# Optimization experiments

Hardware: AMD Instinct MI355X
Metric: run time of the kernel (lower is better)

The kernel has to match this reference:

```python
import jax, jax.numpy as jnp
import numpy as np

N, E, P, D = 100000, 800000, 100000, 128

def setup_inputs() -> dict:
    key = jax.random.key(0)
    ks = jax.random.split(key, 24)
    def w(k, i, o):
        return jax.random.normal(k, (i, o), jnp.float32) * (1.0 / np.sqrt(i))
    inp = {
        'x': jax.random.normal(ks[0], (N, D), jnp.float32),
        'src': jax.random.randint(ks[1], (E,), 0, N, jnp.int32),
        'dst': jax.random.randint(ks[2], (E,), 0, N, jnp.int32),
        'pos_src': jax.random.randint(ks[3], (P,), 0, N, jnp.int32),
        'pos_dst': jax.random.randint(ks[4], (P,), 0, N, jnp.int32),
        'neg_src': jax.random.randint(ks[5], (P,), 0, N, jnp.int32),
        'neg_dst': jax.random.randint(ks[6], (P,), 0, N, jnp.int32),
        # SAGEConv params: fc_self, fc_neigh (+bias) per layer
        'Ws0': w(ks[7], D, D), 'Wn0': w(ks[8], D, D), 'b0': jnp.zeros((D,), jnp.float32),
        'Ws1': w(ks[9], D, D), 'Wn1': w(ks[10], D, D), 'b1': jnp.zeros((D,), jnp.float32),
        'Ws2': w(ks[11], D, D), 'Wn2': w(ks[12], D, D), 'b2': jnp.zeros((D,), jnp.float32),
        # predictor MLP: D->D->D->2
        'Wp0': w(ks[13], D, D), 'bp0': jnp.zeros((D,), jnp.float32),
        'Wp1': w(ks[14], D, D), 'bp1': jnp.zeros((D,), jnp.float32),
        'Wp2': w(ks[15], D, 2), 'bp2': jnp.zeros((2,), jnp.float32),
    }
    return inp

def _sage_layer(h, src, dst, n, Ws, Wn, b, act):
    # mean aggregation over in-neighbors (gather -> segment_sum -> divide)
    msum = jax.ops.segment_sum(h[src], dst, num_segments=n)      # [N, D]
    deg = jax.ops.segment_sum(jnp.ones_like(dst, jnp.float32), dst, num_segments=n)
    h_neigh = msum / jnp.maximum(deg, 1.0)[:, None]
    out = h @ Ws + h_neigh @ Wn + b
    return jax.nn.relu(out) if act else out

def _predict(hs, hd, Wp0, bp0, Wp1, bp1, Wp2, bp2):
    z = hs * hd
    z = jax.nn.relu(z @ Wp0 + bp0)
    z = jax.nn.relu(z @ Wp1 + bp1)
    return jax.nn.softmax(z @ Wp2 + bp2, axis=1)[:, 1]

def reference(x, src, dst, pos_src, pos_dst, neg_src, neg_dst,
              Ws0, Wn0, b0, Ws1, Wn1, b1, Ws2, Wn2, b2,
              Wp0, bp0, Wp1, bp1, Wp2, bp2):
    n = x.shape[0]
    h = _sage_layer(x, src, dst, n, Ws0, Wn0, b0, True)
    h = _sage_layer(h, src, dst, n, Ws1, Wn1, b1, True)
    h = _sage_layer(h, src, dst, n, Ws2, Wn2, b2, False)
    pos = _predict(h[pos_src], h[pos_dst], Wp0, bp0, Wp1, bp1, Wp2, bp2)
    neg = _predict(h[neg_src], h[neg_dst], Wp0, bp0, Wp1, bp1, Wp2, bp2)
    return (pos, neg)
```

## Files before the change

### kernel.cpp

```cpp
#include <hip/hip_runtime.h>
#include <cstdint>
#include <cstddef>
#include <cmath>

#define D 128

typedef short bf16x8 __attribute__((ext_vector_type(8)));
typedef float f32x4 __attribute__((ext_vector_type(4)));

__device__ __forceinline__ ushort f2b(float f) {
  uint x = __float_as_uint(f);
  uint r = ((x >> 16) & 1u) + 0x7fffu;
  return (ushort)((x + r) >> 16);
}
__device__ __forceinline__ float b2f(ushort u) {
  return __uint_as_float(((uint)u) << 16);
}

__global__ __launch_bounds__(256) void k_degree_p(const int* __restrict__ dst, int E,
    int* __restrict__ deg, float scale, int CE) {
  int part = blockIdx.x & 7, chunk = blockIdx.x >> 3;
  long base = (long)chunk * CE;
  for (int i = threadIdx.x; i < CE; i += 256) {
    long e = base + i;
    if (e < E) {
      int d = dst[e];
      int p = (int)((float)d * scale); if (p > 7) p = 7;
      if (p == part) atomicAdd(&deg[d], 1);
    }
  }
}

__global__ __launch_bounds__(256) void k_fill_p(const int* __restrict__ src,
    const int* __restrict__ dst, int E, int* __restrict__ cursor,
    int* __restrict__ csrc, float scale, int CE) {
  int part = blockIdx.x & 7, chunk = blockIdx.x >> 3;
  long base = (long)chunk * CE;
  for (int i = threadIdx.x; i < CE; i += 256) {
    long e = base + i;
    if (e < E) {
      int d = dst[e];
      int p = (int)((float)d * scale); if (p > 7) p = 7;
      if (p == part) {
        int s = src[e];
        int pos = atomicAdd(&cursor[d], 1);
        csrc[pos] = s;
      }
    }
  }
}

#define SCAN_T 256
#define SCAN_E 4
#define SCAN_CHUNK (SCAN_T * SCAN_E)

__global__ void k_scan_partial(const int* __restrict__ deg, int n, int* __restrict__ part) {
  __shared__ int s[SCAN_T];
  int base = blockIdx.x * SCAN_CHUNK;
  int sum = 0;
  for (int i = 0; i < SCAN_E; ++i) {
    int idx = base + (int)threadIdx.x * SCAN_E + i;
    if (idx < n) sum += deg[idx];
  }
  s[threadIdx.x] = sum; __syncthreads();
  for (int ofs = SCAN_T / 2; ofs > 0; ofs >>= 1) {
    if ((int)threadIdx.x < ofs) s[threadIdx.x] += s[threadIdx.x + ofs];
    __syncthreads();
  }
  if (threadIdx.x == 0) part[blockIdx.x] = s[0];
}

__global__ void k_scan_part_ex(int* __restrict__ part, int nb) {
  __shared__ int s[1024];
  int v = ((int)threadIdx.x < nb) ? part[threadIdx.x] : 0;
  s[threadIdx.x] = v; __syncthreads();
  for (int ofs = 1; ofs < 1024; ofs <<= 1) {
    int t = ((int)threadIdx.x >= ofs) ? s[threadIdx.x - ofs] : 0;
    __syncthreads();
    s[threadIdx.x] += t;
    __syncthreads();
  }
  if ((int)threadIdx.x < nb) part[threadIdx.x] = s[threadIdx.x] - v;
}

__global__ void k_scan_final(const int* __restrict__ deg, int n, const int* __restrict__ part,
                             int* __restrict__ rowptr, int E) {
  __shared__ int s[SCAN_T];
  int base = blockIdx.x * SCAN_CHUNK;
  int v[SCAN_E]; int local = 0;
  for (int i = 0; i < SCAN_E; ++i) {
    int idx = base + (int)threadIdx.x * SCAN_E + i;
    v[i] = (idx < n) ? deg[idx] : 0;
    local += v[i];
  }
  s[threadIdx.x] = local; __syncthreads();
  for (int ofs = 1; ofs < SCAN_T; ofs <<= 1) {
    int t = ((int)threadIdx.x >= ofs) ? s[threadIdx.x - ofs] : 0;
    __syncthreads();
    s[threadIdx.x] += t;
    __syncthreads();
  }
  int run = part[blockIdx.x] + s[threadIdx.x] - local;
  for (int i = 0; i < SCAN_E; ++i) {
    int idx = base + (int)threadIdx.x * SCAN_E + i;
    if (idx < n) rowptr[idx] = run;
    run += v[i];
  }
  if (blockIdx.x == 0 && threadIdx.x == 0) rowptr[n] = E;
}

__global__ void k_conv_bf16(const float* __restrict__ in, ushort* __restrict__ out, int n8) {
  int i = blockIdx.x * 256 + threadIdx.x;
  if (i >= n8) return;
  float4 a = ((const float4*)in)[i * 2];
  float4 b = ((const float4*)in)[i * 2 + 1];
  ushort4 o0 = {f2b(a.x), f2b(a.y), f2b(a.z), f2b(a.w)};
  ushort4 o1 = {f2b(b.x), f2b(b.y), f2b(b.z), f2b(b.w)};
  ((ushort4*)out)[i * 2] = o0;
  ((ushort4*)out)[i * 2 + 1] = o1;
}

__global__ void k_pack_all(
    const float* __restrict__ Ws0, const float* __restrict__ Wn0,
    const float* __restrict__ Ws1, const float* __restrict__ Wn1,
    const float* __restrict__ Ws2, const float* __restrict__ Wn2,
    const float* __restrict__ Wp0, const float* __restrict__ Wp1,
    ushort* __restrict__ BpL0, ushort* __restrict__ BpL1, ushort* __restrict__ BpL2,
    ushort* __restrict__ BpP0, ushort* __restrict__ BpP1) {
  int o = blockIdx.x * 256 + threadIdx.x;
  const float *W0, *W1; ushort* out; int rel;
  if (o < 32768)       { W0 = Ws0; W1 = Wn0; out = BpL0; rel = o; }
  else if (o < 65536)  { W0 = Ws1; W1 = Wn1; out = BpL1; rel = o - 32768; }
  else if (o < 98304)  { W0 = Ws2; W1 = Wn2; out = BpL2; rel = o - 65536; }
  else if (o < 114688) { W0 = Wp0; W1 = Wp0; out = BpP0; rel = o - 98304; }
  else                 { W0 = Wp1; W1 = Wp1; out = BpP1; rel = o - 114688; }
  int j = rel & 7, lane = (rel >> 3) & 63, t = (rel >> 9) & 7, ks = rel >> 12;
  int k = ks * 32 + ((lane >> 4) * 8) + j;
  int n = t * 16 + (lane & 15);
  const float* W = (k < 128) ? W0 : W1;
  int kk = (k < 128) ? k : k - 128;
  out[rel] = f2b(W[(size_t)kk * D + n]);
}

#define SMS 136
__global__ __launch_bounds__(256) void k_sage_fused(
    const ushort* __restrict__ A, const int* __restrict__ rowptr,
    const int* __restrict__ csrc, const ushort* __restrict__ Bp,
    const float* __restrict__ bias, ushort* __restrict__ out, int N, int do_relu) {
  __shared__ __align__(16) ushort smean[4][16][SMS];
  int tid = threadIdx.x, wave = tid >> 6, lane = tid & 63;
  int m = lane & 15, kg = lane >> 4;
  int row0 = blockIdx.x * 64 + wave * 16;
  int rp = 0;
  { int idx = row0 + lane; if (lane < 17 && idx <= N) rp = rowptr[idx]; }
  const ushort* hb = A + m * 8;
  for (int t = 0; t < 16; ++t) {
    int beg = __shfl(rp, t), end = __shfl(rp, t + 1);
    if (end < beg) end = beg;
    float f[8] = {0.f, 0.f, 0.f, 0.f, 0.f, 0.f, 0.f, 0.f};
    int i = beg + kg;
    for (; i + 4 < end; i += 8) {
      int s0 = csrc[i], s1 = csrc[i + 4];
      bf16x8 v0 = *(const bf16x8*)(hb + (size_t)s0 * D);
      bf16x8 v1 = *(const bf16x8*)(hb + (size_t)s1 * D);
      #pragma unroll
      for (int j = 0; j < 8; ++j)
        f[j] += b2f((ushort)v0[j]) + b2f((ushort)v1[j]);
    }
    if (i < end) {
      int s0 = csrc[i];
      bf16x8 v0 = *(const bf16x8*)(hb + (size_t)s0 * D);
      #pragma unroll
      for (int j = 0; j < 8; ++j) f[j] += b2f((ushort)v0[j]);
    }
    #pragma unroll
    for (int j = 0; j < 8; ++j) {
      f[j] += __shfl_xor(f[j], 16);
      f[j] += __shfl_xor(f[j], 32);
    }
    if (kg == 0) {
      float inv = (end > beg) ? (1.0f / (float)(end - beg)) : 0.0f;
      bf16x8 o;
      #pragma unroll
      for (int j = 0; j < 8; ++j) o[j] = (short)f2b(f[j] * inv);
      *(bf16x8*)&smean[wave][t][m * 8] = o;
    }
  }
  __syncthreads();
  int ar = row0 + m; if (ar >= N) ar = N - 1;
  const ushort* a_self = A + (size_t)ar * D + kg * 8;
  f32x4 acc[8];
  #pragma unroll
  for (int t = 0; t < 8; ++t) acc[t] = f32x4{0.f, 0.f, 0.f, 0.f};
  #pragma unroll
  for (int ks = 0; ks < 8; ++ks) {
    bf16x8 af = (ks < 4) ? *(const bf16x8*)(a_self + ks * 32)
                         : *(const bf16x8*)&smean[wave][m][(ks - 4) * 32 + kg * 8];
    const ushort* bb = Bp + (size_t)ks * 4096 + lane * 8;
    #pragma unroll
    for (int t = 0; t < 8; ++t)
      acc[t] = __builtin_amdgcn_mfma_f32_16x16x32_bf16(af, *(const bf16x8*)(bb + t * 512), acc[t], 0, 0, 0);
  }
  #pragma unroll
  for (int t = 0; t < 8; ++t) {
    int c = t * 16 + m;
    float bv = bias[c];
    #pragma unroll
    for (int i = 0; i < 4; ++i) {
      int r = row0 + kg * 4 + i;
      float v = acc[t][i] + bv;
      if (do_relu) v = fmaxf(v, 0.f);
      if (r < N) out[(size_t)r * D + c] = f2b(v);
    }
  }
}

__global__ __launch_bounds__(256) void k_predict_mfma(
    const ushort* __restrict__ h,
    const int* __restrict__ ps, const int* __restrict__ pd,
    const int* __restrict__ ns, const int* __restrict__ nd,
    const ushort* __restrict__ Bp0, const float* __restrict__ bp0,
    const ushort* __restrict__ Bp1, const float* __restrict__ bp1,
    const float* __restrict__ Wp2, const float* __restrict__ bp2,
    float* __restrict__ outp, int P, int pb) {
  __shared__ __align__(16) ushort z1p[4][2048];
  int bi = blockIdx.x;
  const int* sidx; const int* didx; float* op;
  if (bi >= pb) { sidx = ns; didx = nd; op = outp + P; bi -= pb; }
  else          { sidx = ps; didx = pd; op = outp; }
  int tid = threadIdx.x;
  int wave = tid >> 6, lane = tid & 63;
  int m = lane & 15, kg = lane >> 4;
  int pair0 = bi * 64 + wave * 16;
  int prow = pair0 + m; int pr = (prow < P) ? prow : P - 1;
  int si = sidx[pr], di = didx[pr];
  const ushort* hs = h + (size_t)si * D + kg * 8;
  const ushort* hd = h + (size_t)di * D + kg * 8;
  f32x4 acc[8];
  #pragma unroll
  for (int t = 0; t < 8; ++t) acc[t] = f32x4{0.f, 0.f, 0.f, 0.f};
  #pragma unroll
  for (int ks = 0; ks < 4; ++ks) {
    bf16x8 as8 = *(const bf16x8*)(hs + ks * 32);
    bf16x8 ad8 = *(const bf16x8*)(hd + ks * 32);
    bf16x8 af;
    #pragma unroll
    for (int j = 0; j < 8; ++j) {
      float p = b2f((ushort)as8[j]) * b2f((ushort)ad8[j]);
      af[j] = (short)f2b(p);
    }
    const ushort* bb = Bp0 + (size_t)ks * 4096 + lane * 8;
    #pragma unroll
    for (int t = 0; t < 8; ++t)
      acc[t] = __builtin_amdgcn_mfma_f32_16x16x32_bf16(af, *(const bf16x8*)(bb + t * 512), acc[t], 0, 0, 0);
  }
  ushort* zp = &z1p[wave][0];
  #pragma unroll
  for (int t = 0; t < 8; ++t) {
    int c = t * 16 + m;
    float bv = bp0[c];
    int ks2 = c >> 5, kg2 = (c >> 3) & 3, j2 = c & 7;
    #pragma unroll
    for (int i = 0; i < 4; ++i) {
      float v = fmaxf(acc[t][i] + bv, 0.f);
      int l2 = kg2 * 16 + kg * 4 + i;
      zp[(ks2 * 64 + l2) * 8 + j2] = f2b(v);
    }
  }
  __syncthreads();
  #pragma unroll
  for (int t = 0; t < 8; ++t) acc[t] = f32x4{0.f, 0.f, 0.f, 0.f};
  #pragma unroll
  for (int ks = 0; ks < 4; ++ks) {
    bf16x8 af = *(const bf16x8*)(zp + (ks * 64 + lane) * 8);
    const ushort* bb = Bp1 + (size_t)ks * 4096 + lane * 8;
    #pragma unroll
    for (int t = 0; t < 8; ++t)
      acc[t] = __builtin_amdgcn_mfma_f32_16x16x32_bf16(af, *(const bf16x8*)(bb + t * 512), acc[t], 0, 0, 0);
  }
  float p0[4] = {0.f, 0.f, 0.f, 0.f}, p1[4] = {0.f, 0.f, 0.f, 0.f};
  #pragma unroll
  for (int t = 0; t < 8; ++t) {
    int c = t * 16 + m;
    float bv = bp1[c];
    float wa = Wp2[(size_t)c * 2], wb = Wp2[(size_t)c * 2 + 1];
    #pragma unroll
    for (int i = 0; i < 4; ++i) {
      float z = fmaxf(acc[t][i] + bv, 0.f);
      p0[i] += z * wa;
      p1[i] += z * wb;
    }
  }
  #pragma unroll
  for (int msk = 1; msk <= 8; msk <<= 1) {
    #pragma unroll
    for (int i = 0; i < 4; ++i) {
      p0[i] += __shfl_xor(p0[i], msk);
      p1[i] += __shfl_xor(p1[i], msk);
    }
  }
  if (m == 0) {
    float c0 = bp2[0], c1 = bp2[1];
    #pragma unroll
    for (int i = 0; i < 4; ++i) {
      int r = pair0 + kg * 4 + i;
      if (r < P) {
        float l0 = p0[i] + c0, l1 = p1[i] + c1;
        op[r] = 1.0f / (1.0f + expf(l0 - l1));
      }
    }
  }
}

extern "C" void kernel_launch(void* const* d_in, const int* in_sizes, int n_in,
                              void* d_out, int out_size, void* d_ws, size_t ws_size,
                              hipStream_t stream) {
  const float* x       = (const float*)d_in[0];
  const int*   src     = (const int*)d_in[1];
  const int*   dst     = (const int*)d_in[2];
  const int*   pos_src = (const int*)d_in[3];
  const int*   pos_dst = (const int*)d_in[4];
  const int*   neg_src = (const int*)d_in[5];
  const int*   neg_dst = (const int*)d_in[6];
  const float* Ws0 = (const float*)d_in[7],  *Wn0 = (const float*)d_in[8],  *b0 = (const float*)d_in[9];
  const float* Ws1 = (const float*)d_in[10], *Wn1 = (const float*)d_in[11], *b1 = (const float*)d_in[12];
  const float* Ws2 = (const float*)d_in[13], *Wn2 = (const float*)d_in[14], *b2 = (const float*)d_in[15];
  const float* Wp0 = (const float*)d_in[16], *bp0 = (const float*)d_in[17];
  const float* Wp1 = (const float*)d_in[18], *bp1 = (const float*)d_in[19];
  const float* Wp2 = (const float*)d_in[20], *bp2 = (const float*)d_in[21];
  const int N = in_sizes[0] / D;
  const int E = in_sizes[1];
  const int P = in_sizes[3];
  float* outp = (float*)d_out;

  char* ws = (char*)d_ws;
  size_t off = 0;
  auto alloc = [&](size_t bytes) -> void* {
    void* p = ws + off;
    off += (bytes + 255) & ~(size_t)255;
    return p;
  };
  ushort* xb    = (ushort*)alloc((size_t)N * D * 2);
  ushort* h1    = (ushort*)alloc((size_t)N * D * 2);
  ushort* h2    = (ushort*)alloc((size_t)N * D * 2);
  ushort* BpL0  = (ushort*)alloc(256 * D * 2);
  ushort* BpL1  = (ushort*)alloc(256 * D * 2);
  ushort* BpL2  = (ushort*)alloc(256 * D * 2);
  ushort* BpP0  = (ushort*)alloc(128 * D * 2);
  ushort* BpP1  = (ushort*)alloc(128 * D * 2);
  int*    deg    = (int*)alloc((size_t)N * 4);
  int*    rowptr = (int*)alloc((size_t)(N + 1) * 4);
  int*    cursor = (int*)alloc((size_t)N * 4);
  int*    part   = (int*)alloc(4096);
  int*    csrc   = (int*)alloc((size_t)E * 4);
  (void)ws_size; (void)n_in; (void)out_size;

  const float pscale = 8.0f / (float)N;
  const int CB = 96;
  const int CE = (E + CB - 1) / CB;

  hipMemsetAsync(deg, 0, (size_t)N * 4, stream);
  k_degree_p<<<8 * CB, 256, 0, stream>>>(dst, E, deg, pscale, CE);
  int nb = (N + SCAN_CHUNK - 1) / SCAN_CHUNK;
  k_scan_partial<<<nb, SCAN_T, 0, stream>>>(deg, N, part);
  k_scan_part_ex<<<1, 1024, 0, stream>>>(part, nb);
  k_scan_final<<<nb, SCAN_T, 0, stream>>>(deg, N, part, rowptr, E);
  hipMemcpyAsync(cursor, rowptr, (size_t)N * 4, hipMemcpyDeviceToDevice, stream);
  k_fill_p<<<8 * CB, 256, 0, stream>>>(src, dst, E, cursor, csrc, pscale, CE);

  int n8 = N * D / 8;
  k_conv_bf16<<<(n8 + 255) / 256, 256, 0, stream>>>(x, xb, n8);
  k_pack_all<<<512, 256, 0, stream>>>(Ws0, Wn0, Ws1, Wn1, Ws2, Wn2, Wp0, Wp1,
                                      BpL0, BpL1, BpL2, BpP0, BpP1);

  int gemb = (N + 63) / 64;
  k_sage_fused<<<gemb, 256, 0, stream>>>(xb, rowptr, csrc, BpL0, b0, h1, N, 1);
  k_sage_fused<<<gemb, 256, 0, stream>>>(h1, rowptr, csrc, BpL1, b1, h2, N, 1);
  k_sage_fused<<<gemb, 256, 0, stream>>>(h2, rowptr, csrc, BpL2, b2, xb, N, 0);

  int pb = (P + 63) / 64;
  k_predict_mfma<<<2 * pb, 256, 0, stream>>>(xb, pos_src, pos_dst, neg_src, neg_dst,
                                             BpP0, bp0, BpP1, bp1, Wp2, bp2, outp, P, pb);
}
```

Before: 498.0 us.

## Remap neighbor aggregation to 16-lane groups per node and fuse cursor init

The gather phase of the fused SAGE kernel now assigns each 16-thread group to four nodes in turn. Each group accumulates all of a node's edges itself with a 4-way unrolled load loop, so the per-node cross-lane shuffle reduction goes away. Previously each wave walked 16 nodes one after another, splitting edges across four lane groups. Separately, the scan kernel now writes the cursor array directly, which replaces a device-to-device memcpy. The new mapping lets 16 nodes per wave proceed concurrently, but degree imbalance between nodes in the same wave may cause divergence.

```diff
diff --git a/kernel.cpp b/kernel.cpp
--- a/kernel.cpp
+++ b/kernel.cpp
@@ -84,7 +84,7 @@
 }
 
 __global__ void k_scan_final(const int* __restrict__ deg, int n, const int* __restrict__ part,
-                             int* __restrict__ rowptr, int E) {
+                             int* __restrict__ rowptr, int* __restrict__ cursor, int E) {
   __shared__ int s[SCAN_T];
   int base = blockIdx.x * SCAN_CHUNK;
   int v[SCAN_E]; int local = 0;
@@ -103,7 +103,7 @@
   int run = part[blockIdx.x] + s[threadIdx.x] - local;
   for (int i = 0; i < SCAN_E; ++i) {
     int idx = base + (int)threadIdx.x * SCAN_E + i;
-    if (idx < n) rowptr[idx] = run;
+    if (idx < n) { rowptr[idx] = run; cursor[idx] = run; }
     run += v[i];
   }
   if (blockIdx.x == 0 && threadIdx.x == 0) rowptr[n] = E;
@@ -147,46 +147,44 @@
     const ushort* __restrict__ A, const int* __restrict__ rowptr,
     const int* __restrict__ csrc, const ushort* __restrict__ Bp,
     const float* __restrict__ bias, ushort* __restrict__ out, int N, int do_relu) {
-  __shared__ __align__(16) ushort smean[4][16][SMS];
+  __shared__ __align__(16) ushort smean[64][SMS];
   int tid = threadIdx.x, wave = tid >> 6, lane = tid & 63;
   int m = lane & 15, kg = lane >> 4;
-  int row0 = blockIdx.x * 64 + wave * 16;
-  int rp = 0;
-  { int idx = row0 + lane; if (lane < 17 && idx <= N) rp = rowptr[idx]; }
-  const ushort* hb = A + m * 8;
-  for (int t = 0; t < 16; ++t) {
-    int beg = __shfl(rp, t), end = __shfl(rp, t + 1);
-    if (end < beg) end = beg;
+  int g = tid >> 4, sub = tid & 15;
+  const ushort* hb = A + sub * 8;
+  #pragma unroll
+  for (int j = 0; j < 4; ++j) {
+    int r = g * 4 + j;
+    int node = blockIdx.x * 64 + r;
+    int beg = 0, end = 0;
+    if (node < N) { beg = rowptr[node]; end = rowptr[node + 1]; }
     float f[8] = {0.f, 0.f, 0.f, 0.f, 0.f, 0.f, 0.f, 0.f};
-    int i = beg + kg;
-    for (; i + 4 < end; i += 8) {
-      int s0 = csrc[i], s1 = csrc[i + 4];
+    int i = beg;
+    for (; i + 3 < end; i += 4) {
+      int s0 = csrc[i], s1 = csrc[i + 1], s2 = csrc[i + 2], s3 = csrc[i + 3];
       bf16x8 v0 = *(const bf16x8*)(hb + (size_t)s0 * D);
       bf16x8 v1 = *(const bf16x8*)(hb + (size_t)s1 * D);
+      bf16x8 v2 = *(const bf16x8*)(hb + (size_t)s2 * D);
+      bf16x8 v3 = *(const bf16x8*)(hb + (size_t)s3 * D);
       #pragma unroll
-      for (int j = 0; j < 8; ++j)
-        f[j] += b2f((ushort)v0[j]) + b2f((ushort)v1[j]);
-    }
-    if (i < end) {
+      for (int q = 0; q < 8; ++q)
+        f[q] += (b2f((ushort)v0[q]) + b2f((ushort)v1[q]))
+              + (b2f((ushort)v2[q]) + b2f((ushort)v3[q]));
+    }
+    for (; i < end; ++i) {
       int s0 = csrc[i];
       bf16x8 v0 = *(const bf16x8*)(hb + (size_t)s0 * D);
       #pragma unroll
-      for (int j = 0; j < 8; ++j) f[j] += b2f((ushort)v0[j]);
-    }
-    #pragma unroll
-    for (int j = 0; j < 8; ++j) {
-      f[j] += __shfl_xor(f[j], 16);
-      f[j] += __shfl_xor(f[j], 32);
-    }
-    if (kg == 0) {
-      float inv = (end > beg) ? (1.0f / (float)(end - beg)) : 0.0f;
-      bf16x8 o;
-      #pragma unroll
-      for (int j = 0; j < 8; ++j) o[j] = (short)f2b(f[j] * inv);
-      *(bf16x8*)&smean[wave][t][m * 8] = o;
-    }
+      for (int q = 0; q < 8; ++q) f[q] += b2f((ushort)v0[q]);
+    }
+    float inv = (end > beg) ? (1.0f / (float)(end - beg)) : 0.0f;
+    bf16x8 o;
+    #pragma unroll
+    for (int q = 0; q < 8; ++q) o[q] = (short)f2b(f[q] * inv);
+    *(bf16x8*)&smean[r][sub * 8] = o;
   }
   __syncthreads();
+  int row0 = blockIdx.x * 64 + wave * 16;
   int ar = row0 + m; if (ar >= N) ar = N - 1;
   const ushort* a_self = A + (size_t)ar * D + kg * 8;
   f32x4 acc[8];
@@ -195,7 +193,7 @@
   #pragma unroll
   for (int ks = 0; ks < 8; ++ks) {
     bf16x8 af = (ks < 4) ? *(const bf16x8*)(a_self + ks * 32)
-                         : *(const bf16x8*)&smean[wave][m][(ks - 4) * 32 + kg * 8];
+                         : *(const bf16x8*)&smean[wave * 16 + m][(ks - 4) * 32 + kg * 8];
     const ushort* bb = Bp + (size_t)ks * 4096 + lane * 8;
     #pragma unroll
     for (int t = 0; t < 8; ++t)
@@ -364,8 +362,7 @@
   int nb = (N + SCAN_CHUNK - 1) / SCAN_CHUNK;
   k_scan_partial<<<nb, SCAN_T, 0, stream>>>(deg, N, part);
   k_scan_part_ex<<<1, 1024, 0, stream>>>(part, nb);
-  k_scan_final<<<nb, SCAN_T, 0, stream>>>(deg, N, part, rowptr, E);
-  hipMemcpyAsync(cursor, rowptr, (size_t)N * 4, hipMemcpyDeviceToDevice, stream);
+  k_scan_final<<<nb, SCAN_T, 0, stream>>>(deg, N, part, rowptr, cursor, E);
   k_fill_p<<<8 * CB, 256, 0, stream>>>(src, dst, E, cursor, csrc, pscale, CE);
 
   int n8 = N * D / 8;
```

New measurement: 468.1 us. 1.06x faster.
